# Optimization experiments

Measured on AMD Instinct MI355X. Metric: run time of the kernel, lower is better.

Reference implementation:

```python
import math
import jax, jax.numpy as jnp
import numpy as np

D = 256       # d_model
R = 64        # low-rank bottleneck
E = 3         # num experts
KS = (1, 3, 5)
EPS = 0.1     # sinkhorn epsilon
ITERS = 10    # sinkhorn iterations


def _ln(x, g, b):
    m = jnp.mean(x, -1, keepdims=True)
    v = jnp.mean((x - m) ** 2, -1, keepdims=True)
    return (x - m) * jax.lax.rsqrt(v + 1e-5) * g + b


def _gelu(x):
    return jax.nn.gelu(x, approximate=False)  # torch nn.GELU default (erf)


def setup_inputs() -> dict:
    key = jax.random.key(0)
    ks = jax.random.split(key, 12)
    s = 0.02
    B, Lt, La = 16, 1024, 2048
    return {
        "text_feat": jax.random.normal(ks[0], (B, Lt, D), jnp.float32),
        "audio_feat": jax.random.normal(ks[1], (B, La, D), jnp.float32),
        # shared OT projection (LayerNorm + Linear, shared across modalities)
        "ln_g": jnp.ones((D,), jnp.float32),
        "ln_b": jnp.zeros((D,), jnp.float32),
        "W_sh": jax.random.normal(ks[2], (D, D), jnp.float32) * s,
        "b_sh": jnp.zeros((D,), jnp.float32),
        # contradiction router: Linear(d+1->d) GELU Linear(d->E)
        "Wr1": jax.random.normal(ks[3], (D, D + 1), jnp.float32) * s,
        "br1": jnp.zeros((D,), jnp.float32),
        "Wr2": jax.random.normal(ks[4], (E, D), jnp.float32) * s,
        "br2": jnp.zeros((E,), jnp.float32),
        # 3 low-rank conv experts (stacked where shapes match)
        "down_W": jax.random.normal(ks[5], (E, R, D), jnp.float32) * s,
        "down_b": jnp.zeros((E, R), jnp.float32),
        "conv_w1": jax.random.normal(ks[6], (R, R, 1), jnp.float32) * s,
        "conv_w3": jax.random.normal(ks[7], (R, R, 3), jnp.float32) * s,
        "conv_w5": jax.random.normal(ks[8], (R, R, 5), jnp.float32) * s,
        "conv_b": jnp.zeros((E, R), jnp.float32),
        "up_W": jax.random.normal(ks[9], (E, D, R), jnp.float32) * s,
        "up_b": jnp.zeros((E, D), jnp.float32),
        "en_g": jnp.ones((E, D), jnp.float32),
        "en_b": jnp.zeros((E, D), jnp.float32),
    }


def reference(text_feat, audio_feat, ln_g, ln_b, W_sh, b_sh, Wr1, br1, Wr2, br2,
              down_W, down_b, conv_w1, conv_w3, conv_w5, conv_b, up_W, up_b, en_g, en_b):
    B, Lt, _ = text_feat.shape
    La = audio_feat.shape[1]

    # ---- shared projection (dropout = identity at eval) ----
    Tp = _ln(text_feat, ln_g, ln_b) @ W_sh.T + b_sh      # [B,Lt,D]
    Ap = _ln(audio_feat, ln_g, ln_b) @ W_sh.T + b_sh     # [B,La,D]

    # ---- cosine cost ----
    Tn = Tp / jnp.maximum(jnp.linalg.norm(Tp, axis=-1, keepdims=True), 1e-12)
    An = Ap / jnp.maximum(jnp.linalg.norm(Ap, axis=-1, keepdims=True), 1e-12)
    cost = 1.0 - jnp.einsum('bmd,bnd->bmn', Tn, An)      # [B,Lt,La]

    # ---- log-domain Sinkhorn (uniform marginals, no masks) ----
    log_K = -cost / (EPS + 1e-8)
    log_mu = jnp.full((B, Lt), -math.log(Lt), jnp.float32)
    log_nu = jnp.full((B, La), -math.log(La), jnp.float32)
    lu = jnp.zeros((B, Lt), jnp.float32)
    lv = jnp.zeros((B, La), jnp.float32)
    for _ in range(ITERS):
        lu = log_mu - jax.scipy.special.logsumexp(log_K + lv[:, None, :], axis=-1)
        lu = jnp.nan_to_num(jnp.clip(lu, -1e9, 1e9), nan=0.0, posinf=1e9, neginf=-1e9)
        lv = log_nu - jax.scipy.special.logsumexp(log_K + lu[:, :, None], axis=1)
        lv = jnp.nan_to_num(jnp.clip(lv, -1e9, 1e9), nan=0.0, posinf=1e9, neginf=-1e9)
    pi = jnp.exp(lu[:, :, None] + log_K + lv[:, None, :])
    pi = jnp.nan_to_num(pi, nan=0.0, posinf=1.0, neginf=0.0)  # [B,Lt,La]

    A_al = jnp.einsum('bmn,bnd->bmd', pi, Ap)            # [B,Lt,D]
    S = jnp.sum(Tp * A_al, -1)                           # [B,Lt]
    resid = jnp.abs(Tp - A_al)                           # [B,Lt,D]

    # ---- contradiction router ----
    rin = jnp.concatenate([S[..., None], resid], -1)     # [B,Lt,D+1]
    G = jax.nn.softmax(_gelu(rin @ Wr1.T + br1) @ Wr2.T + br2, axis=-1)  # [B,Lt,E]

    # ---- multi-scale low-rank conv MoE over contradiction residual ----
    convs = (conv_w1, conv_w3, conv_w5)
    x = resid
    out = jnp.zeros_like(Tp)
    for e in range(E):
        h = _gelu(x @ down_W[e].T + down_b[e])           # [B,Lt,R]
        k = convs[e].shape[-1]
        pad = (k - 1) // 2
        hc = jax.lax.conv_general_dilated(
            h.transpose(0, 2, 1), convs[e], (1,), [(pad, pad)],
            dimension_numbers=('NCH', 'OIH', 'NCH')) + conv_b[e][None, :, None]
        h = _gelu(hc).transpose(0, 2, 1)                 # [B,Lt,R]
        h = h @ up_W[e].T + up_b[e]                      # [B,Lt,D]
        eo = _ln(h + x, en_g[e], en_b[e])
        out = out + G[..., e:e + 1] * eo
    return out
```

## Files before the change

kernel.cpp:

```cpp
#include <hip/hip_runtime.h>
#include <cstdio>

#define D_ 256
#define LT 1024
#define LA 2048
#define NB 16
#define RR_ 64
#define NRT (NB*LT)
#define NRA (NB*LA)

#define DECQ  (-0.080645161f)
#define DECQ2 (-0.11634637f)

typedef short bf16x8 __attribute__((ext_vector_type(8)));
typedef float f32x4 __attribute__((ext_vector_type(4)));

__device__ __forceinline__ float gelu_f(float x) {
    return 0.5f * x * (1.0f + erff(x * 0.70710678118654752f));
}
__device__ __forceinline__ unsigned short f2bf(float f) {
    union { float f; unsigned int i; } c; c.f = f;
    unsigned int x = c.i;
    return (unsigned short)((x + 0x7fffu + ((x >> 16) & 1u)) >> 16);
}

__global__ __launch_bounds__(256) void k_prep_all(
    const float* __restrict__ W_sh, const float* __restrict__ down_W,
    const float* __restrict__ up_W, const float* __restrict__ Wr1,
    unsigned short* __restrict__ Wb, unsigned short* __restrict__ dWb,
    unsigned short* __restrict__ uWb, unsigned short* __restrict__ Wr1b)
{
    int i = blockIdx.x * 256 + threadIdx.x;
    if (i < 65536) Wb[i] = f2bf(W_sh[i]);
    else if (i < 114688) { int j = i - 65536; dWb[j] = f2bf(down_W[j]); }
    else if (i < 163840) { int j = i - 114688; uWb[j] = f2bf(up_W[j]); }
    else { int j = i - 163840; int n = j >> 8, k = j & 255; Wr1b[j] = f2bf(Wr1[(long)n * 257 + 1 + k]); }
}

__global__ __launch_bounds__(256) void k_lnproj_mfma(
    const float* __restrict__ X, const float* __restrict__ g, const float* __restrict__ bln,
    const unsigned short* __restrict__ Wb, const float* __restrict__ bsh,
    float* __restrict__ Pf, unsigned short* __restrict__ Nb)
{
    __shared__ short xb[64][264];
    __shared__ short Bs[256][40];
    int tid = threadIdx.x;
    long row0 = (long)blockIdx.x * 64;
    {
        int lane = tid & 31, rg = tid >> 5;
        float4 ga = *(const float4*)(g + lane * 8);
        float4 gb2 = *(const float4*)(g + lane * 8 + 4);
        float4 ba = *(const float4*)(bln + lane * 8);
        float4 bb2 = *(const float4*)(bln + lane * 8 + 4);
        for (int it = 0; it < 8; it++) {
            int r = it * 8 + rg;
            const float4* xp4 = (const float4*)(X + (row0 + r) * D_);
            float4 a = xp4[lane * 2], b = xp4[lane * 2 + 1];
            float s = a.x + a.y + a.z + a.w + b.x + b.y + b.z + b.w;
#pragma unroll
            for (int off = 16; off >= 1; off >>= 1) s += __shfl_xor(s, off);
            float mean = s * (1.0f / 256.0f);
            float q = (a.x - mean) * (a.x - mean) + (a.y - mean) * (a.y - mean)
                    + (a.z - mean) * (a.z - mean) + (a.w - mean) * (a.w - mean)
                    + (b.x - mean) * (b.x - mean) + (b.y - mean) * (b.y - mean)
                    + (b.z - mean) * (b.z - mean) + (b.w - mean) * (b.w - mean);
#pragma unroll
            for (int off = 16; off >= 1; off >>= 1) q += __shfl_xor(q, off);
            float ivar = rsqrtf(q * (1.0f / 256.0f) + 1e-5f);
            unsigned int u0 = f2bf((a.x - mean) * ivar * ga.x + ba.x);
            unsigned int u1 = f2bf((a.y - mean) * ivar * ga.y + ba.y);
            unsigned int u2 = f2bf((a.z - mean) * ivar * ga.z + ba.z);
            unsigned int u3 = f2bf((a.w - mean) * ivar * ga.w + ba.w);
            unsigned int u4 = f2bf((b.x - mean) * ivar * gb2.x + bb2.x);
            unsigned int u5 = f2bf((b.y - mean) * ivar * gb2.y + bb2.y);
            unsigned int u6 = f2bf((b.z - mean) * ivar * gb2.z + bb2.z);
            unsigned int u7 = f2bf((b.w - mean) * ivar * gb2.w + bb2.w);
            int4 pv;
            pv.x = (int)(u0 | (u1 << 16)); pv.y = (int)(u2 | (u3 << 16));
            pv.z = (int)(u4 | (u5 << 16)); pv.w = (int)(u6 | (u7 << 16));
            *(int4*)&xb[r][lane * 8] = pv;
        }
    }
    __syncthreads();
    int wid = tid >> 6, lane = tid & 63;
    int l15 = lane & 15, kq = lane >> 4;
    int m_local = wid * 16;
    f32x4 acc[16];
#pragma unroll
    for (int j = 0; j < 16; j++) acc[j] = (f32x4){0.f, 0.f, 0.f, 0.f};
    for (int kt = 0; kt < 8; kt++) {
        int k0 = kt * 32;
#pragma unroll
        for (int h = 0; h < 4; h++) {
            int idx = tid + 256 * h;
            int n = idx >> 2, qc = idx & 3;
            *(int4*)&Bs[n][qc * 8] = *(const int4*)(Wb + (long)n * D_ + k0 + qc * 8);
        }
        __syncthreads();
        bf16x8 af = *(const bf16x8*)&xb[m_local + l15][k0 + kq * 8];
#pragma unroll
        for (int j = 0; j < 16; j++) {
            bf16x8 bf = *(const bf16x8*)&Bs[j * 16 + l15][kq * 8];
            acc[j] = __builtin_amdgcn_mfma_f32_16x16x32_bf16(af, bf, acc[j], 0, 0, 0);
        }
        __syncthreads();
    }
#pragma unroll
    for (int j = 0; j < 16; j++) {
        float bv = bsh[j * 16 + l15];
#pragma unroll
        for (int r = 0; r < 4; r++) acc[j][r] += bv;
    }
    float sq[4] = {0.f, 0.f, 0.f, 0.f};
#pragma unroll
    for (int j = 0; j < 16; j++)
#pragma unroll
        for (int r = 0; r < 4; r++) sq[r] += acc[j][r] * acc[j][r];
#pragma unroll
    for (int off = 8; off >= 1; off >>= 1) {
#pragma unroll
        for (int r = 0; r < 4; r++) sq[r] += __shfl_xor(sq[r], off);
    }
    float rinv[4];
#pragma unroll
    for (int r = 0; r < 4; r++) rinv[r] = 1.0f / fmaxf(sqrtf(sq[r]), 1e-12f);
#pragma unroll
    for (int j = 0; j < 16; j++) {
        int col = j * 16 + l15;
#pragma unroll
        for (int r = 0; r < 4; r++) {
            long m = row0 + m_local + kq * 4 + r;
            if (Pf) Pf[m * D_ + col] = acc[j][r];
            Nb[m * D_ + col] = f2bf(acc[j][r] * rinv[r]);
        }
    }
}

__global__ __launch_bounds__(256) void k_transpose_bf(
    const unsigned short* __restrict__ Anb, unsigned short* __restrict__ ApbT)
{
    __shared__ short t[64][68];
    int b = blockIdx.x;
    int n0 = blockIdx.y * 64;
    int d0 = blockIdx.z * 64;
    int tid = threadIdx.x;
#pragma unroll
    for (int h = 0; h < 2; h++) {
        int c = tid + 256 * h;
        int nr = c >> 3, ch = c & 7;
        *(int4*)&t[nr][ch * 8] = *(const int4*)(Anb + ((long)b * LA + n0 + nr) * D_ + d0 + ch * 8);
    }
    __syncthreads();
#pragma unroll
    for (int h = 0; h < 2; h++) {
        int c = tid + 256 * h;
        int d = c >> 3, nch = c & 7;
        unsigned short v[8];
#pragma unroll
        for (int k = 0; k < 8; k++) v[k] = (unsigned short)t[nch * 8 + k][d];
        int4 ov;
        ov.x = (int)((unsigned int)v[0] | ((unsigned int)v[1] << 16));
        ov.y = (int)((unsigned int)v[2] | ((unsigned int)v[3] << 16));
        ov.z = (int)((unsigned int)v[4] | ((unsigned int)v[5] << 16));
        ov.w = (int)((unsigned int)v[6] | ((unsigned int)v[7] << 16));
        *(int4*)(ApbT + ((long)b * D_ + d0 + d) * LA + n0 + nch * 8) = ov;
    }
}

__global__ __launch_bounds__(256) void k_cost_mfma(
    const unsigned short* __restrict__ Tnb, const unsigned short* __restrict__ Anb,
    unsigned char* __restrict__ logK8, unsigned char* __restrict__ logK8T)
{
    __shared__ short sm[2][128][48];
    short (*As)[48] = sm[0];
    short (*Bs)[48] = sm[1];
    unsigned char* tile = (unsigned char*)sm;
    int b = blockIdx.x;
    int m_blk = blockIdx.y * 128, n_blk = blockIdx.z * 128;
    int tid = threadIdx.x;
    int wid = tid >> 6, lane = tid & 63;
    int l15 = lane & 15, kq = lane >> 4;
    int wm0 = (wid >> 1) * 64, wn0 = (wid & 1) * 64;
    const unsigned short* Ab = Tnb + ((long)b * LT + m_blk) * D_;
    const unsigned short* Bb = Anb + ((long)b * LA + n_blk) * D_;
    f32x4 acc[4][4];
#pragma unroll
    for (int i = 0; i < 4; i++)
#pragma unroll
        for (int j = 0; j < 4; j++) acc[i][j] = (f32x4){0.f, 0.f, 0.f, 0.f};
    for (int kt = 0; kt < 8; kt++) {
        int k0 = kt * 32;
#pragma unroll
        for (int h = 0; h < 2; h++) {
            int idx = tid + 256 * h;
            int row = idx >> 2, ch = idx & 3;
            *(int4*)&As[row][ch * 8] = *(const int4*)(Ab + (long)row * D_ + k0 + ch * 8);
            *(int4*)&Bs[row][ch * 8] = *(const int4*)(Bb + (long)row * D_ + k0 + ch * 8);
        }
        __syncthreads();
        bf16x8 af[4], bfv[4];
#pragma unroll
        for (int i = 0; i < 4; i++) af[i] = *(const bf16x8*)&As[wm0 + i * 16 + l15][kq * 8];
#pragma unroll
        for (int j = 0; j < 4; j++) bfv[j] = *(const bf16x8*)&Bs[wn0 + j * 16 + l15][kq * 8];
#pragma unroll
        for (int i = 0; i < 4; i++)
#pragma unroll
            for (int j = 0; j < 4; j++)
                acc[i][j] = __builtin_amdgcn_mfma_f32_16x16x32_bf16(af[i], bfv[j], acc[i][j], 0, 0, 0);
        __syncthreads();
    }
#pragma unroll
    for (int i = 0; i < 4; i++) {
#pragma unroll
        for (int j = 0; j < 4; j++) {
            int n = wn0 + j * 16 + l15;
            long base = ((long)b * LT + m_blk + wm0 + i * 16 + kq * 4) * (long)LA + n_blk + n;
            unsigned int pk = 0;
#pragma unroll
            for (int r = 0; r < 4; r++) {
                float q = rintf((1.0f - acc[i][j][r]) * 124.0f);
                q = fminf(fmaxf(q, 0.0f), 255.0f);
                unsigned int qb = (unsigned int)q;
                pk |= qb << (8 * r);
                logK8[base + (long)r * LA] = (unsigned char)qb;
            }
            *(unsigned int*)&tile[n * 144 + wm0 + i * 16 + kq * 4] = pk;
        }
    }
    __syncthreads();
#pragma unroll
    for (int h = 0; h < 4; h++) {
        int idx = tid + 256 * h;
        int row = idx >> 3, ch = idx & 7;
        int4 v = *(const int4*)&tile[row * 144 + ch * 16];
        *(int4*)(logK8T + ((long)b * LA + n_blk + row) * (long)LT + m_blk + ch * 16) = v;
    }
}

__global__ __launch_bounds__(256) void k_rowlse2(
    const unsigned char* __restrict__ logK8, const float* __restrict__ lv2,
    float* __restrict__ lu2, int first)
{
    __shared__ float red[8][4];
    int b = blockIdx.x & 15;
    int mseg = blockIdx.x >> 4;
    int tid = threadIdx.x;
    int wid = tid >> 6, lane = tid & 63;
    float lvv[8] = {0.f, 0.f, 0.f, 0.f, 0.f, 0.f, 0.f, 0.f};
    if (!first) {
        const float* lvp = lv2 + (long)b * LA + tid * 8;
        float4 l0 = *(const float4*)lvp, l1 = *(const float4*)(lvp + 4);
        lvv[0] = l0.x; lvv[1] = l0.y; lvv[2] = l0.z; lvv[3] = l0.w;
        lvv[4] = l1.x; lvv[5] = l1.y; lvv[6] = l1.z; lvv[7] = l1.w;
    }
    const unsigned char* p = logK8 + ((long)b * LT + mseg * 8) * (long)LA + tid * 8;
#pragma unroll
    for (int r = 0; r < 8; r++) {
        uint2 w = *(const uint2*)(p + (long)r * LA);
        unsigned int w0 = w.x, w1 = w.y;
        float s = 0.f;
        s += exp2f(fmaf((float)(w0 & 0xffu),         DECQ2, lvv[0]));
        s += exp2f(fmaf((float)((w0 >> 8) & 0xffu),  DECQ2, lvv[1]));
        s += exp2f(fmaf((float)((w0 >> 16) & 0xffu), DECQ2, lvv[2]));
        s += exp2f(fmaf((float)(w0 >> 24),           DECQ2, lvv[3]));
        s += exp2f(fmaf((float)(w1 & 0xffu),         DECQ2, lvv[4]));
        s += exp2f(fmaf((float)((w1 >> 8) & 0xffu),  DECQ2, lvv[5]));
        s += exp2f(fmaf((float)((w1 >> 16) & 0xffu), DECQ2, lvv[6]));
        s += exp2f(fmaf((float)(w1 >> 24),           DECQ2, lvv[7]));
#pragma unroll
        for (int off = 32; off >= 1; off >>= 1) s += __shfl_xor(s, off);
        if (lane == 0) red[r][wid] = s;
    }
    __syncthreads();
    if (tid < 8) {
        float s = red[tid][0] + red[tid][1] + red[tid][2] + red[tid][3];
        lu2[(long)b * LT + mseg * 8 + tid] = -10.0f - __log2f(s);
    }
}

__global__ __launch_bounds__(256) void k_collse2(
    const unsigned char* __restrict__ logK8T, const float* __restrict__ lu2,
    float* __restrict__ lv2, int final_)
{
    __shared__ float red[16][2];
    int b = blockIdx.x & 15;
    int nseg = blockIdx.x >> 4;
    int tid = threadIdx.x;
    int t7 = tid & 127;
    int g = tid >> 7;
    int wid = tid >> 6, lane = tid & 63;
    const float* lup = lu2 + (long)b * LT + t7 * 8;
    float4 l0 = *(const float4*)lup, l1 = *(const float4*)(lup + 4);
    float lus[8] = {l0.x, l0.y, l0.z, l0.w, l1.x, l1.y, l1.z, l1.w};
    const unsigned char* base = logK8T + ((long)b * LA + nseg * 16) * (long)LT + t7 * 8;
#pragma unroll
    for (int it = 0; it < 8; it++) {
        int c = it * 2 + g;
        uint2 w = *(const uint2*)(base + (long)c * LT);
        unsigned int w0 = w.x, w1 = w.y;
        float s = 0.f;
        s += exp2f(fmaf((float)(w0 & 0xffu),         DECQ2, lus[0]));
        s += exp2f(fmaf((float)((w0 >> 8) & 0xffu),  DECQ2, lus[1]));
        s += exp2f(fmaf((float)((w0 >> 16) & 0xffu), DECQ2, lus[2]));
        s += exp2f(fmaf((float)(w0 >> 24),           DECQ2, lus[3]));
        s += exp2f(fmaf((float)(w1 & 0xffu),         DECQ2, lus[4]));
        s += exp2f(fmaf((float)((w1 >> 8) & 0xffu),  DECQ2, lus[5]));
        s += exp2f(fmaf((float)((w1 >> 16) & 0xffu), DECQ2, lus[6]));
        s += exp2f(fmaf((float)(w1 >> 24),           DECQ2, lus[7]));
#pragma unroll
        for (int off = 32; off >= 1; off >>= 1) s += __shfl_xor(s, off);
        if (lane == 0) red[c][wid & 1] = s;
    }
    __syncthreads();
    if (tid < 16) {
        float s = red[tid][0] + red[tid][1];
        lv2[(long)b * LA + nseg * 16 + tid] = final_ ? (0.00048828125f / s)
                                                     : (-11.0f - __log2f(s));
    }
}

__global__ __launch_bounds__(256) void k_scale_ev(
    unsigned short* __restrict__ ApbT, const float* __restrict__ ev)
{
    int b = blockIdx.x;
    int d = blockIdx.y;
    int tid = threadIdx.x;
    long off = ((long)b * D_ + d) * (long)LA + tid * 8;
    int4 v = *(const int4*)(ApbT + off);
    const float* ep = ev + (long)b * LA + tid * 8;
    float4 e0 = *(const float4*)ep, e1 = *(const float4*)(ep + 4);
    unsigned int u[4] = {(unsigned int)v.x, (unsigned int)v.y, (unsigned int)v.z, (unsigned int)v.w};
    float ee[8] = {e0.x, e0.y, e0.z, e0.w, e1.x, e1.y, e1.z, e1.w};
    unsigned int o[4];
#pragma unroll
    for (int k = 0; k < 4; k++) {
        float lo = __uint_as_float(u[k] << 16) * ee[2 * k];
        float hi = __uint_as_float(u[k] & 0xffff0000u) * ee[2 * k + 1];
        o[k] = (unsigned int)f2bf(lo) | ((unsigned int)f2bf(hi) << 16);
    }
    int4 ov; ov.x = (int)o[0]; ov.y = (int)o[1]; ov.z = (int)o[2]; ov.w = (int)o[3];
    *(int4*)(ApbT + off) = ov;
}

__global__ __launch_bounds__(256) void k_pi2(
    const unsigned char* __restrict__ logK8, const unsigned short* __restrict__ Av,
    const float* __restrict__ lu2, float* __restrict__ Apart)
{
    __shared__ short As[64][48];
    __shared__ short Bs[256][48];
    __shared__ float eus[64];
    int b = blockIdx.x;
    int kh = blockIdx.y;
    int m_blk = blockIdx.z * 64;
    int nbase = kh * 1024;
    int tid = threadIdx.x;
    if (tid < 64) eus[tid] = exp2f(lu2[(long)b * LT + m_blk + tid]);
    int wid = tid >> 6, lane = tid & 63;
    int l15 = lane & 15, kq = lane >> 4;
    int wm0 = (wid & 1) * 32, wd0 = (wid >> 1) * 128;
    f32x4 acc[2][8];
#pragma unroll
    for (int i = 0; i < 2; i++)
#pragma unroll
        for (int j = 0; j < 8; j++) acc[i][j] = (f32x4){0.f, 0.f, 0.f, 0.f};
    const unsigned char* Kbase = logK8 + ((long)b * LT + m_blk) * (long)LA + nbase;
    const unsigned short* Bbase = Av + (long)b * D_ * (long)LA + nbase;
    int arow = tid >> 2, ac8 = (tid & 3) * 8;
    for (int kt = 0; kt < 32; kt++) {
        int n0 = kt * 32;
        {
            uint2 raw = *(const uint2*)(Kbase + (long)arow * LA + n0 + ac8);
            unsigned int w0 = raw.x, w1 = raw.y;
            unsigned int o0 = f2bf(exp2f((float)(w0 & 0xffu) * DECQ2));
            unsigned int o1 = f2bf(exp2f((float)((w0 >> 8) & 0xffu) * DECQ2));
            unsigned int o2 = f2bf(exp2f((float)((w0 >> 16) & 0xffu) * DECQ2));
            unsigned int o3 = f2bf(exp2f((float)(w0 >> 24) * DECQ2));
            unsigned int o4 = f2bf(exp2f((float)(w1 & 0xffu) * DECQ2));
            unsigned int o5 = f2bf(exp2f((float)((w1 >> 8) & 0xffu) * DECQ2));
            unsigned int o6 = f2bf(exp2f((float)((w1 >> 16) & 0xffu) * DECQ2));
            unsigned int o7 = f2bf(exp2f((float)(w1 >> 24) * DECQ2));
            int4 ov;
            ov.x = (int)(o0 | (o1 << 16)); ov.y = (int)(o2 | (o3 << 16));
            ov.z = (int)(o4 | (o5 << 16)); ov.w = (int)(o6 | (o7 << 16));
            *(int4*)&As[arow][ac8] = ov;
        }
#pragma unroll
        for (int h = 0; h < 4; h++) {
            int idx = tid + 256 * h;
            int row = idx >> 2, ch = idx & 3;
            *(int4*)&Bs[row][ch * 8] = *(const int4*)(Bbase + (long)row * LA + n0 + ch * 8);
        }
        __syncthreads();
        bf16x8 af[2], bfv[8];
        af[0] = *(const bf16x8*)&As[wm0 + l15][kq * 8];
        af[1] = *(const bf16x8*)&As[wm0 + 16 + l15][kq * 8];
#pragma unroll
        for (int j = 0; j < 8; j++) bfv[j] = *(const bf16x8*)&Bs[wd0 + j * 16 + l15][kq * 8];
#pragma unroll
        for (int i = 0; i < 2; i++)
#pragma unroll
            for (int j = 0; j < 8; j++)
                acc[i][j] = __builtin_amdgcn_mfma_f32_16x16x32_bf16(af[i], bfv[j], acc[i][j], 0, 0, 0);
        __syncthreads();
    }
    float* dst = Apart + (long)kh * (NB * (long)LT * D_);
#pragma unroll
    for (int i = 0; i < 2; i++) {
#pragma unroll
        for (int r = 0; r < 4; r++) {
            int rloc = wm0 + i * 16 + kq * 4 + r;
            float eu = eus[rloc];
            int m = m_blk + rloc;
            long obase = ((long)b * LT + m) * D_;
#pragma unroll
            for (int j = 0; j < 8; j++)
                dst[obase + wd0 + j * 16 + l15] = acc[i][j][r] * eu;
        }
    }
}

__global__ __launch_bounds__(256) void k_sresid(
    const float* __restrict__ Tp, const float* __restrict__ Apart,
    float* __restrict__ resid, unsigned short* __restrict__ residb, float* __restrict__ S)
{
    __shared__ float red[4];
    int b = blockIdx.x & 15;
    int m = blockIdx.x >> 4;
    long row = (long)b * LT + m;
    int tid = threadIdx.x;
    long idx = row * D_ + tid;
    float t = Tp[idx];
    float a = Apart[idx] + Apart[idx + (long)NB * LT * D_];
    float rr = fabsf(t - a);
    resid[idx] = rr;
    residb[idx] = f2bf(rr);
    float p = t * a;
#pragma unroll
    for (int off = 32; off >= 1; off >>= 1) p += __shfl_xor(p, off);
    if ((tid & 63) == 0) red[tid >> 6] = p;
    __syncthreads();
    if (tid == 0) S[row] = red[0] + red[1] + red[2] + red[3];
}

__global__ __launch_bounds__(256) void k_router_fused(
    const unsigned short* __restrict__ residb, const unsigned short* __restrict__ Wr1b,
    const float* __restrict__ Wr1, const float* __restrict__ br1,
    const float* __restrict__ S, const float* __restrict__ Wr2,
    const float* __restrict__ br2, float* __restrict__ G)
{
    __shared__ short xb[16][264];
    __shared__ short Bs[256][40];
    __shared__ float red[4][3][16];
    int tid = threadIdx.x;
    long row0 = (long)blockIdx.x * 16;
#pragma unroll
    for (int h = 0; h < 2; h++) {
        int idx = tid + 256 * h;
        int row = idx >> 5, ch = idx & 31;
        *(int4*)&xb[row][ch * 8] = *(const int4*)(residb + (row0 + row) * D_ + ch * 8);
    }
    __syncthreads();
    int wid = tid >> 6, lane = tid & 63;
    int l15 = lane & 15, kq = lane >> 4;
    f32x4 acc[4];
#pragma unroll
    for (int j = 0; j < 4; j++) acc[j] = (f32x4){0.f, 0.f, 0.f, 0.f};
    for (int kt = 0; kt < 8; kt++) {
        int k0 = kt * 32;
#pragma unroll
        for (int h = 0; h < 4; h++) {
            int idx = tid + 256 * h;
            int n = idx >> 2, qc = idx & 3;
            *(int4*)&Bs[n][qc * 8] = *(const int4*)(Wr1b + (long)n * D_ + k0 + qc * 8);
        }
        __syncthreads();
        bf16x8 af = *(const bf16x8*)&xb[l15][k0 + kq * 8];
#pragma unroll
        for (int j = 0; j < 4; j++) {
            bf16x8 bf = *(const bf16x8*)&Bs[wid * 64 + j * 16 + l15][kq * 8];
            acc[j] = __builtin_amdgcn_mfma_f32_16x16x32_bf16(af, bf, acc[j], 0, 0, 0);
        }
        __syncthreads();
    }
    float sv[4];
#pragma unroll
    for (int r = 0; r < 4; r++) sv[r] = S[row0 + kq * 4 + r];
    float le[3][4] = {};
#pragma unroll
    for (int j = 0; j < 4; j++) {
        int col = wid * 64 + j * 16 + l15;
        float w0 = Wr1[(long)col * 257];
        float bv = br1[col];
        float w2a = Wr2[col], w2b = Wr2[256 + col], w2c = Wr2[512 + col];
#pragma unroll
        for (int r = 0; r < 4; r++) {
            float hv = gelu_f(acc[j][r] + sv[r] * w0 + bv);
            le[0][r] += hv * w2a;
            le[1][r] += hv * w2b;
            le[2][r] += hv * w2c;
        }
    }
#pragma unroll
    for (int off = 8; off >= 1; off >>= 1)
#pragma unroll
        for (int e = 0; e < 3; e++)
#pragma unroll
            for (int r = 0; r < 4; r++) le[e][r] += __shfl_xor(le[e][r], off);
    if (l15 == 0) {
#pragma unroll
        for (int e = 0; e < 3; e++)
#pragma unroll
            for (int r = 0; r < 4; r++) red[wid][e][kq * 4 + r] = le[e][r];
    }
    __syncthreads();
    if (tid < 16) {
        float L0 = red[0][0][tid] + red[1][0][tid] + red[2][0][tid] + red[3][0][tid] + br2[0];
        float L1 = red[0][1][tid] + red[1][1][tid] + red[2][1][tid] + red[3][1][tid] + br2[1];
        float L2 = red[0][2][tid] + red[1][2][tid] + red[2][2][tid] + red[3][2][tid] + br2[2];
        float mx = fmaxf(L0, fmaxf(L1, L2));
        float e0 = __expf(L0 - mx), e1 = __expf(L1 - mx), e2 = __expf(L2 - mx);
        float inv = 1.0f / (e0 + e1 + e2);
        long m = row0 + tid;
        G[m] = e0 * inv; G[NRT + m] = e1 * inv; G[2 * NRT + m] = e2 * inv;
    }
}

__global__ __launch_bounds__(256) void k_down_mfma(
    const unsigned short* __restrict__ residb, const unsigned short* __restrict__ dWb,
    const float* __restrict__ db, float* __restrict__ hall)
{
    __shared__ short xb[64][264];
    __shared__ short Bs[64][40];
    int tid = threadIdx.x;
    int e = blockIdx.y;
    int b = blockIdx.x & 15;
    int mseg = blockIdx.x >> 4;
    long row0 = (long)b * LT + mseg * 64;
    const unsigned short* dWe = dWb + (long)e * RR_ * D_;
    float* h = hall + (long)e * NRT * RR_;
#pragma unroll
    for (int hh = 0; hh < 8; hh++) {
        int idx = tid + 256 * hh;
        int row = idx >> 5, ch = idx & 31;
        *(int4*)&xb[row][ch * 8] = *(const int4*)(residb + (row0 + row) * D_ + ch * 8);
    }
    __syncthreads();
    int wid = tid >> 6, lane = tid & 63;
    int l15 = lane & 15, kq = lane >> 4;
    int m_local = wid * 16;
    f32x4 acc[4];
#pragma unroll
    for (int j = 0; j < 4; j++) acc[j] = (f32x4){0.f, 0.f, 0.f, 0.f};
    for (int kt = 0; kt < 8; kt++) {
        int k0 = kt * 32;
        {
            int n = tid >> 2, qc = tid & 3;
            *(int4*)&Bs[n][qc * 8] = *(const int4*)(dWe + (long)n * D_ + k0 + qc * 8);
        }
        __syncthreads();
        bf16x8 af = *(const bf16x8*)&xb[m_local + l15][k0 + kq * 8];
#pragma unroll
        for (int j = 0; j < 4; j++) {
            bf16x8 bf = *(const bf16x8*)&Bs[j * 16 + l15][kq * 8];
            acc[j] = __builtin_amdgcn_mfma_f32_16x16x32_bf16(af, bf, acc[j], 0, 0, 0);
        }
        __syncthreads();
    }
#pragma unroll
    for (int j = 0; j < 4; j++) {
        int col = j * 16 + l15;
        float bv = db[e * RR_ + col];
#pragma unroll
        for (int r = 0; r < 4; r++) {
            long m = row0 + m_local + kq * 4 + r;
            h[m * RR_ + col] = gelu_f(acc[j][r] + bv);
        }
    }
}

__global__ __launch_bounds__(256) void k_conv_all(
    const float* __restrict__ hall, const float* __restrict__ cw1,
    const float* __restrict__ cw3, const float* __restrict__ cw5,
    const float* __restrict__ conv_b, unsigned short* __restrict__ hcbb)
{
    __shared__ float hs[68][68];
    __shared__ float wt[64][64];
    int e = blockIdx.y;
    const float* w = (e == 0) ? cw1 : ((e == 1) ? cw3 : cw5);
    int ksz = (e == 0) ? 1 : ((e == 1) ? 3 : 5);
    const float* h = hall + (long)e * NRT * RR_;
    unsigned short* hcb = hcbb + (long)e * NRT * RR_;
    const float* cb = conv_b + e * 64;
    int b = blockIdx.x & 15;
    int m0 = (blockIdx.x >> 4) * 64;
    int tid = threadIdx.x;
    int pad = (ksz - 1) >> 1;
    for (int idx = tid; idx < 68 * 16; idx += 256) {
        int mr = idx >> 4, i4 = idx & 15;
        int mm = m0 - 2 + mr;
        float4 vv = { 0.f, 0.f, 0.f, 0.f };
        if (mm >= 0 && mm < LT) vv = *(const float4*)(h + ((long)b * LT + mm) * RR_ + i4 * 4);
        *(float4*)&hs[mr][i4 * 4] = vv;
    }
    int tx = tid & 15, ty = tid >> 4;
    float acc[4][4] = {};
    for (int t = 0; t < ksz; t++) {
        __syncthreads();
        for (int idx = tid; idx < 4096; idx += 256) {
            int i = idx & 63, j = idx >> 6;
            wt[i][j] = w[(long)j * RR_ * ksz + i * ksz + t];
        }
        __syncthreads();
        int roff = ty * 4 + 2 + t - pad;
        for (int i4 = 0; i4 < 16; i4++) {
            float4 h0 = *(const float4*)&hs[roff + 0][i4 * 4];
            float4 h1 = *(const float4*)&hs[roff + 1][i4 * 4];
            float4 h2 = *(const float4*)&hs[roff + 2][i4 * 4];
            float4 h3 = *(const float4*)&hs[roff + 3][i4 * 4];
            float hh[4][4] = { { h0.x, h0.y, h0.z, h0.w }, { h1.x, h1.y, h1.z, h1.w },
                               { h2.x, h2.y, h2.z, h2.w }, { h3.x, h3.y, h3.z, h3.w } };
#pragma unroll
            for (int s = 0; s < 4; s++) {
                float4 wv = *(const float4*)&wt[i4 * 4 + s][tx * 4];
#pragma unroll
                for (int r = 0; r < 4; r++) {
                    acc[r][0] += hh[r][s] * wv.x;
                    acc[r][1] += hh[r][s] * wv.y;
                    acc[r][2] += hh[r][s] * wv.z;
                    acc[r][3] += hh[r][s] * wv.w;
                }
            }
        }
    }
    float4 bb = *(const float4*)(cb + tx * 4);
#pragma unroll
    for (int r = 0; r < 4; r++) {
        long m = (long)b * LT + m0 + ty * 4 + r;
        unsigned long long pv =
              (unsigned long long)f2bf(gelu_f(acc[r][0] + bb.x))
            | ((unsigned long long)f2bf(gelu_f(acc[r][1] + bb.y)) << 16)
            | ((unsigned long long)f2bf(gelu_f(acc[r][2] + bb.z)) << 32)
            | ((unsigned long long)f2bf(gelu_f(acc[r][3] + bb.w)) << 48);
        *(unsigned long long*)(hcb + m * RR_ + tx * 4) = pv;
    }
}

__global__ __launch_bounds__(256) void k_up3(
    const unsigned short* __restrict__ hcbb, const unsigned short* __restrict__ uWb,
    const float* __restrict__ up_b, const float* __restrict__ resid,
    const float* __restrict__ en_g, const float* __restrict__ en_b,
    const float* __restrict__ G, float* __restrict__ out)
{
    __shared__ short hs[64][88];
    __shared__ short Bs[256][40];
    int tid = threadIdx.x;
    int b = blockIdx.x & 15;
    int mseg = blockIdx.x >> 4;
    long row0 = (long)b * LT + mseg * 64;
    int wid = tid >> 6, lane = tid & 63;
    int l15 = lane & 15, kq = lane >> 4;
    int m_local = wid * 16;
    long mrow[4];
#pragma unroll
    for (int r = 0; r < 4; r++) mrow[r] = row0 + m_local + kq * 4 + r;
    f32x4 outacc[16];
#pragma unroll
    for (int j = 0; j < 16; j++) outacc[j] = (f32x4){0.f, 0.f, 0.f, 0.f};
    for (int e = 0; e < 3; e++) {
        __syncthreads();
        const unsigned short* hcb = hcbb + (long)e * NRT * RR_;
        const unsigned short* uWe = uWb + (long)e * 16384;
#pragma unroll
        for (int hh = 0; hh < 2; hh++) {
            int idx = tid + 256 * hh;
            int row = idx >> 3, ch = idx & 7;
            *(int4*)&hs[row][ch * 8] = *(const int4*)(hcb + (row0 + row) * RR_ + ch * 8);
        }
        f32x4 acc[16];
#pragma unroll
        for (int j = 0; j < 16; j++) acc[j] = (f32x4){0.f, 0.f, 0.f, 0.f};
        for (int kt = 0; kt < 2; kt++) {
            int k0 = kt * 32;
#pragma unroll
            for (int hh = 0; hh < 4; hh++) {
                int idx = tid + 256 * hh;
                int n = idx >> 2, qc = idx & 3;
                *(int4*)&Bs[n][qc * 8] = *(const int4*)(uWe + (long)n * RR_ + k0 + qc * 8);
            }
            __syncthreads();
            bf16x8 af = *(const bf16x8*)&hs[m_local + l15][k0 + kq * 8];
#pragma unroll
            for (int j = 0; j < 16; j++) {
                bf16x8 bf = *(const bf16x8*)&Bs[j * 16 + l15][kq * 8];
                acc[j] = __builtin_amdgcn_mfma_f32_16x16x32_bf16(af, bf, acc[j], 0, 0, 0);
            }
            __syncthreads();
        }
        const float* ub = up_b + e * 256;
#pragma unroll
        for (int j = 0; j < 16; j++) {
            int col = j * 16 + l15;
            float bv = ub[col];
#pragma unroll
            for (int r = 0; r < 4; r++)
                acc[j][r] += bv + resid[mrow[r] * D_ + col];
        }
        float s[4] = {0.f, 0.f, 0.f, 0.f};
#pragma unroll
        for (int j = 0; j < 16; j++)
#pragma unroll
            for (int r = 0; r < 4; r++) s[r] += acc[j][r];
#pragma unroll
        for (int off = 8; off >= 1; off >>= 1)
#pragma unroll
            for (int r = 0; r < 4; r++) s[r] += __shfl_xor(s[r], off);
        float mn[4];
#pragma unroll
        for (int r = 0; r < 4; r++) mn[r] = s[r] * (1.0f / 256.0f);
        float q[4] = {0.f, 0.f, 0.f, 0.f};
#pragma unroll
        for (int j = 0; j < 16; j++)
#pragma unroll
            for (int r = 0; r < 4; r++) { float d = acc[j][r] - mn[r]; q[r] += d * d; }
#pragma unroll
        for (int off = 8; off >= 1; off >>= 1)
#pragma unroll
            for (int r = 0; r < 4; r++) q[r] += __shfl_xor(q[r], off);
        float iv[4], gv[4];
#pragma unroll
        for (int r = 0; r < 4; r++) {
            iv[r] = rsqrtf(q[r] * (1.0f / 256.0f) + 1e-5f);
            gv[r] = G[(long)e * NRT + mrow[r]];
        }
        const float* eg = en_g + e * 256;
        const float* eb = en_b + e * 256;
#pragma unroll
        for (int j = 0; j < 16; j++) {
            int col = j * 16 + l15;
            float egc = eg[col], ebc = eb[col];
#pragma unroll
            for (int r = 0; r < 4; r++)
                outacc[j][r] += gv[r] * ((acc[j][r] - mn[r]) * iv[r] * egc + ebc);
        }
    }
#pragma unroll
    for (int j = 0; j < 16; j++) {
        int col = j * 16 + l15;
#pragma unroll
        for (int r = 0; r < 4; r++)
            out[mrow[r] * D_ + col] = outacc[j][r];
    }
}

extern "C" void kernel_launch(void* const* d_in, const int* in_sizes, int n_in,
                              void* d_out, int out_size, void* d_ws, size_t ws_size,
                              hipStream_t stream)
{
    const float* text   = (const float*)d_in[0];
    const float* audio  = (const float*)d_in[1];
    const float* ln_g   = (const float*)d_in[2];
    const float* ln_b   = (const float*)d_in[3];
    const float* W_sh   = (const float*)d_in[4];
    const float* b_sh   = (const float*)d_in[5];
    const float* Wr1    = (const float*)d_in[6];
    const float* br1    = (const float*)d_in[7];
    const float* Wr2    = (const float*)d_in[8];
    const float* br2    = (const float*)d_in[9];
    const float* down_W = (const float*)d_in[10];
    const float* down_b = (const float*)d_in[11];
    const float* cw1    = (const float*)d_in[12];
    const float* cw3    = (const float*)d_in[13];
    const float* cw5    = (const float*)d_in[14];
    const float* conv_b = (const float*)d_in[15];
    const float* up_W   = (const float*)d_in[16];
    const float* up_b   = (const float*)d_in[17];
    const float* en_g   = (const float*)d_in[18];
    const float* en_b   = (const float*)d_in[19];

    float* ws = (float*)d_ws;
    float*          Tp    = ws;
    unsigned short* Tnb   = (unsigned short*)(ws + 4194304);
    unsigned short* Anb   = (unsigned short*)(ws + 6291456);
    unsigned short* ApbT  = (unsigned short*)(ws + 10485760);
    unsigned char*  logK8 = (unsigned char*)(ws + 14680064);
    float*          Apart = ws + 23068672;
    float*          resid = ws + 31457280;
    unsigned short* residb= (unsigned short*)(ws + 35651584);
    float*          lu2   = ws + 37748736;
    float*          lv2   = ws + 37765120;
    float*          Sb    = ws + 37797888;
    float*          Gb    = ws + 37814272;
    unsigned short* Wb    = (unsigned short*)(ws + 37863424);
    unsigned short* dWb   = (unsigned short*)(ws + 37896192);
    unsigned short* uWb   = (unsigned short*)(ws + 37920768);
    unsigned short* Wr1b  = (unsigned short*)(ws + 37945344);
    size_t need_bytes = (size_t)37978112 * 4;
    if (ws_size < need_bytes) {
        fprintf(stderr, "kernel_launch: ws_size %zu < needed %zu\n", ws_size, need_bytes);
        return;
    }
    float*          hall = ws + 14680064;
    unsigned short* hcbb = (unsigned short*)(ws + 17825792);
    unsigned char*  logK8T = (unsigned char*)(ws + 23068672);

    k_prep_all<<<896, 256, 0, stream>>>(W_sh, down_W, up_W, Wr1, Wb, dWb, uWb, Wr1b);
    k_lnproj_mfma<<<NRT / 64, 256, 0, stream>>>(text, ln_g, ln_b, Wb, b_sh, Tp, Tnb);
    k_lnproj_mfma<<<NRA / 64, 256, 0, stream>>>(audio, ln_g, ln_b, Wb, b_sh, nullptr, Anb);
    k_transpose_bf<<<dim3(NB, LA / 64, D_ / 64), 256, 0, stream>>>(Anb, ApbT);
    k_cost_mfma<<<dim3(NB, LT / 128, LA / 128), 256, 0, stream>>>(Tnb, Anb, logK8, logK8T);
    for (int it = 0; it < 10; it++) {
        k_rowlse2<<<NRT / 8, 256, 0, stream>>>(logK8, lv2, lu2, it == 0 ? 1 : 0);
        k_collse2<<<NB * (LA / 16), 256, 0, stream>>>(logK8T, lu2, lv2, it == 9 ? 1 : 0);
    }
    k_scale_ev<<<dim3(NB, D_), 256, 0, stream>>>(ApbT, lv2);
    k_pi2<<<dim3(NB, 2, LT / 64), 256, 0, stream>>>(logK8, ApbT, lu2, Apart);
    k_sresid<<<NRT, 256, 0, stream>>>(Tp, Apart, resid, residb, Sb);
    k_router_fused<<<NRT / 16, 256, 0, stream>>>(residb, Wr1b, Wr1, br1, Sb, Wr2, br2, Gb);
    k_down_mfma<<<dim3(NRT / 64, 3), 256, 0, stream>>>(residb, dWb, down_b, hall);
    k_conv_all<<<dim3(NRT / 64, 3), 256, 0, stream>>>(hall, cw1, cw3, cw5, conv_b, hcbb);
    k_up3<<<NRT / 64, 256, 0, stream>>>(hcbb, uWb, up_b, resid, en_g, en_b, Gb, (float*)d_out);
}
```

Before: 581.6 us.

## Restructure Sinkhorn LSE kernels for more parallelism and use hardware exp2/bf16 pack

The row and column log-sum-exp kernels now give each block fewer rows or columns, 2 rows and 4 columns instead of 8 and 16. Each thread loads 16 bytes with a single vector load, so the grid has more blocks and more loads are in flight. exp2f is replaced with the raw v_exp_f32 builtin and the software bf16 rounding with v_cvt_pk_bf16_f32 in the scale and pi kernels. The LDS row stride in k_pi2 is padded from 48 to 56 to change the bank-conflict pattern. The fast exp skips denormal handling, and the extra blocks mean lv2/lu2 vectors are re-read more times.

```diff
diff --git a/kernel.cpp b/kernel.cpp
--- a/kernel.cpp
+++ b/kernel.cpp
@@ -22,6 +22,18 @@
     union { float f; unsigned int i; } c; c.f = f;
     unsigned int x = c.i;
     return (unsigned short)((x + 0x7fffu + ((x >> 16) & 1u)) >> 16);
+}
+__device__ __forceinline__ float exp2_fast(float x) {
+#if __has_builtin(__builtin_amdgcn_exp2f)
+    return __builtin_amdgcn_exp2f(x);
+#else
+    float r; asm("v_exp_f32 %0, %1" : "=v"(r) : "v"(x)); return r;
+#endif
+}
+__device__ __forceinline__ unsigned int cvt_pk_bf16(float lo, float hi) {
+    unsigned int r;
+    asm("v_cvt_pk_bf16_f32 %0, %1, %2" : "=v"(r) : "v"(lo), "v"(hi));
+    return r;
 }
 
 __global__ __launch_bounds__(256) void k_prep_all(
@@ -238,85 +250,85 @@
     }
 }
 
-__global__ __launch_bounds__(256) void k_rowlse2(
+__global__ __launch_bounds__(256) void k_rowlse3(
     const unsigned char* __restrict__ logK8, const float* __restrict__ lv2,
     float* __restrict__ lu2, int first)
 {
-    __shared__ float red[8][4];
+    __shared__ float red[2][2];
     int b = blockIdx.x & 15;
     int mseg = blockIdx.x >> 4;
     int tid = threadIdx.x;
-    int wid = tid >> 6, lane = tid & 63;
-    float lvv[8] = {0.f, 0.f, 0.f, 0.f, 0.f, 0.f, 0.f, 0.f};
+    int row = tid >> 7;
+    int ln = tid & 127;
+    float lvv[16];
     if (!first) {
-        const float* lvp = lv2 + (long)b * LA + tid * 8;
-        float4 l0 = *(const float4*)lvp, l1 = *(const float4*)(lvp + 4);
-        lvv[0] = l0.x; lvv[1] = l0.y; lvv[2] = l0.z; lvv[3] = l0.w;
-        lvv[4] = l1.x; lvv[5] = l1.y; lvv[6] = l1.z; lvv[7] = l1.w;
-    }
-    const unsigned char* p = logK8 + ((long)b * LT + mseg * 8) * (long)LA + tid * 8;
-#pragma unroll
-    for (int r = 0; r < 8; r++) {
-        uint2 w = *(const uint2*)(p + (long)r * LA);
-        unsigned int w0 = w.x, w1 = w.y;
-        float s = 0.f;
-        s += exp2f(fmaf((float)(w0 & 0xffu),         DECQ2, lvv[0]));
-        s += exp2f(fmaf((float)((w0 >> 8) & 0xffu),  DECQ2, lvv[1]));
-        s += exp2f(fmaf((float)((w0 >> 16) & 0xffu), DECQ2, lvv[2]));
-        s += exp2f(fmaf((float)(w0 >> 24),           DECQ2, lvv[3]));
-        s += exp2f(fmaf((float)(w1 & 0xffu),         DECQ2, lvv[4]));
-        s += exp2f(fmaf((float)((w1 >> 8) & 0xffu),  DECQ2, lvv[5]));
-        s += exp2f(fmaf((float)((w1 >> 16) & 0xffu), DECQ2, lvv[6]));
-        s += exp2f(fmaf((float)(w1 >> 24),           DECQ2, lvv[7]));
-#pragma unroll
-        for (int off = 32; off >= 1; off >>= 1) s += __shfl_xor(s, off);
-        if (lane == 0) red[r][wid] = s;
-    }
+        const float* lvp = lv2 + (long)b * LA + ln * 16;
+#pragma unroll
+        for (int k = 0; k < 4; k++) {
+            float4 l = *(const float4*)(lvp + k * 4);
+            lvv[k * 4 + 0] = l.x; lvv[k * 4 + 1] = l.y;
+            lvv[k * 4 + 2] = l.z; lvv[k * 4 + 3] = l.w;
+        }
+    } else {
+#pragma unroll
+        for (int k = 0; k < 16; k++) lvv[k] = 0.f;
+    }
+    const unsigned char* p = logK8 + ((long)b * LT + mseg * 2 + row) * (long)LA + ln * 16;
+    uint4 w = *(const uint4*)p;
+    unsigned int ws4[4] = {w.x, w.y, w.z, w.w};
+    float s = 0.f;
+#pragma unroll
+    for (int k = 0; k < 4; k++) {
+        unsigned int u = ws4[k];
+        s += exp2_fast(fmaf((float)(u & 0xffu),         DECQ2, lvv[k * 4 + 0]));
+        s += exp2_fast(fmaf((float)((u >> 8) & 0xffu),  DECQ2, lvv[k * 4 + 1]));
+        s += exp2_fast(fmaf((float)((u >> 16) & 0xffu), DECQ2, lvv[k * 4 + 2]));
+        s += exp2_fast(fmaf((float)(u >> 24),           DECQ2, lvv[k * 4 + 3]));
+    }
+#pragma unroll
+    for (int off = 32; off >= 1; off >>= 1) s += __shfl_xor(s, off);
+    if ((tid & 63) == 0) red[row][(tid >> 6) & 1] = s;
     __syncthreads();
-    if (tid < 8) {
-        float s = red[tid][0] + red[tid][1] + red[tid][2] + red[tid][3];
-        lu2[(long)b * LT + mseg * 8 + tid] = -10.0f - __log2f(s);
-    }
-}
-
-__global__ __launch_bounds__(256) void k_collse2(
+    if (tid < 2) {
+        float sr = red[tid][0] + red[tid][1];
+        lu2[(long)b * LT + mseg * 2 + tid] = -10.0f - __log2f(sr);
+    }
+}
+
+__global__ __launch_bounds__(256) void k_collse3(
     const unsigned char* __restrict__ logK8T, const float* __restrict__ lu2,
     float* __restrict__ lv2, int final_)
 {
-    __shared__ float red[16][2];
     int b = blockIdx.x & 15;
     int nseg = blockIdx.x >> 4;
     int tid = threadIdx.x;
-    int t7 = tid & 127;
-    int g = tid >> 7;
-    int wid = tid >> 6, lane = tid & 63;
-    const float* lup = lu2 + (long)b * LT + t7 * 8;
-    float4 l0 = *(const float4*)lup, l1 = *(const float4*)(lup + 4);
-    float lus[8] = {l0.x, l0.y, l0.z, l0.w, l1.x, l1.y, l1.z, l1.w};
-    const unsigned char* base = logK8T + ((long)b * LA + nseg * 16) * (long)LT + t7 * 8;
-#pragma unroll
-    for (int it = 0; it < 8; it++) {
-        int c = it * 2 + g;
-        uint2 w = *(const uint2*)(base + (long)c * LT);
-        unsigned int w0 = w.x, w1 = w.y;
-        float s = 0.f;
-        s += exp2f(fmaf((float)(w0 & 0xffu),         DECQ2, lus[0]));
-        s += exp2f(fmaf((float)((w0 >> 8) & 0xffu),  DECQ2, lus[1]));
-        s += exp2f(fmaf((float)((w0 >> 16) & 0xffu), DECQ2, lus[2]));
-        s += exp2f(fmaf((float)(w0 >> 24),           DECQ2, lus[3]));
-        s += exp2f(fmaf((float)(w1 & 0xffu),         DECQ2, lus[4]));
-        s += exp2f(fmaf((float)((w1 >> 8) & 0xffu),  DECQ2, lus[5]));
-        s += exp2f(fmaf((float)((w1 >> 16) & 0xffu), DECQ2, lus[6]));
-        s += exp2f(fmaf((float)(w1 >> 24),           DECQ2, lus[7]));
-#pragma unroll
-        for (int off = 32; off >= 1; off >>= 1) s += __shfl_xor(s, off);
-        if (lane == 0) red[c][wid & 1] = s;
-    }
-    __syncthreads();
-    if (tid < 16) {
-        float s = red[tid][0] + red[tid][1];
-        lv2[(long)b * LA + nseg * 16 + tid] = final_ ? (0.00048828125f / s)
-                                                     : (-11.0f - __log2f(s));
+    int wv = tid >> 6, lane = tid & 63;
+    int c = nseg * 4 + wv;
+    float lus[16];
+    const float* lup = lu2 + (long)b * LT + lane * 16;
+#pragma unroll
+    for (int k = 0; k < 4; k++) {
+        float4 l = *(const float4*)(lup + k * 4);
+        lus[k * 4 + 0] = l.x; lus[k * 4 + 1] = l.y;
+        lus[k * 4 + 2] = l.z; lus[k * 4 + 3] = l.w;
+    }
+    const unsigned char* p = logK8T + ((long)b * LA + c) * (long)LT + lane * 16;
+    uint4 w = *(const uint4*)p;
+    unsigned int ws4[4] = {w.x, w.y, w.z, w.w};
+    float s = 0.f;
+#pragma unroll
+    for (int k = 0; k < 4; k++) {
+        unsigned int u = ws4[k];
+        s += exp2_fast(fmaf((float)(u & 0xffu),         DECQ2, lus[k * 4 + 0]));
+        s += exp2_fast(fmaf((float)((u >> 8) & 0xffu),  DECQ2, lus[k * 4 + 1]));
+        s += exp2_fast(fmaf((float)((u >> 16) & 0xffu), DECQ2, lus[k * 4 + 2]));
+        s += exp2_fast(fmaf((float)(u >> 24),           DECQ2, lus[k * 4 + 3]));
+    }
+#pragma unroll
+    for (int off = 32; off >= 1; off >>= 1) s += __shfl_xor(s, off);
+    if (lane == 0) {
+        lv2[(long)b * LA + c] = final_ ? (0.00048828125f / s)
+                                       : (-11.0f - __log2f(s));
     }
 }
 
@@ -337,7 +349,7 @@
     for (int k = 0; k < 4; k++) {
         float lo = __uint_as_float(u[k] << 16) * ee[2 * k];
         float hi = __uint_as_float(u[k] & 0xffff0000u) * ee[2 * k + 1];
-        o[k] = (unsigned int)f2bf(lo) | ((unsigned int)f2bf(hi) << 16);
+        o[k] = cvt_pk_bf16(lo, hi);
     }
     int4 ov; ov.x = (int)o[0]; ov.y = (int)o[1]; ov.z = (int)o[2]; ov.w = (int)o[3];
     *(int4*)(ApbT + off) = ov;
@@ -347,15 +359,15 @@
     const unsigned char* __restrict__ logK8, const unsigned short* __restrict__ Av,
     const float* __restrict__ lu2, float* __restrict__ Apart)
 {
-    __shared__ short As[64][48];
-    __shared__ short Bs[256][48];
+    __shared__ short As[64][56];
+    __shared__ short Bs[256][56];
     __shared__ float eus[64];
     int b = blockIdx.x;
     int kh = blockIdx.y;
     int m_blk = blockIdx.z * 64;
     int nbase = kh * 1024;
     int tid = threadIdx.x;
-    if (tid < 64) eus[tid] = exp2f(lu2[(long)b * LT + m_blk + tid]);
+    if (tid < 64) eus[tid] = exp2_fast(lu2[(long)b * LT + m_blk + tid]);
     int wid = tid >> 6, lane = tid & 63;
     int l15 = lane & 15, kq = lane >> 4;
     int wm0 = (wid & 1) * 32, wd0 = (wid >> 1) * 128;
@@ -372,17 +384,17 @@
         {
             uint2 raw = *(const uint2*)(Kbase + (long)arow * LA + n0 + ac8);
             unsigned int w0 = raw.x, w1 = raw.y;
-            unsigned int o0 = f2bf(exp2f((float)(w0 & 0xffu) * DECQ2));
-            unsigned int o1 = f2bf(exp2f((float)((w0 >> 8) & 0xffu) * DECQ2));
-            unsigned int o2 = f2bf(exp2f((float)((w0 >> 16) & 0xffu) * DECQ2));
-            unsigned int o3 = f2bf(exp2f((float)(w0 >> 24) * DECQ2));
-            unsigned int o4 = f2bf(exp2f((float)(w1 & 0xffu) * DECQ2));
-            unsigned int o5 = f2bf(exp2f((float)((w1 >> 8) & 0xffu) * DECQ2));
-            unsigned int o6 = f2bf(exp2f((float)((w1 >> 16) & 0xffu) * DECQ2));
-            unsigned int o7 = f2bf(exp2f((float)(w1 >> 24) * DECQ2));
+            float e0 = exp2_fast((float)(w0 & 0xffu) * DECQ2);
+            float e1 = exp2_fast((float)((w0 >> 8) & 0xffu) * DECQ2);
+            float e2 = exp2_fast((float)((w0 >> 16) & 0xffu) * DECQ2);
+            float e3 = exp2_fast((float)(w0 >> 24) * DECQ2);
+            float e4 = exp2_fast((float)(w1 & 0xffu) * DECQ2);
+            float e5 = exp2_fast((float)((w1 >> 8) & 0xffu) * DECQ2);
+            float e6 = exp2_fast((float)((w1 >> 16) & 0xffu) * DECQ2);
+            float e7 = exp2_fast((float)(w1 >> 24) * DECQ2);
             int4 ov;
-            ov.x = (int)(o0 | (o1 << 16)); ov.y = (int)(o2 | (o3 << 16));
-            ov.z = (int)(o4 | (o5 << 16)); ov.w = (int)(o6 | (o7 << 16));
+            ov.x = (int)cvt_pk_bf16(e0, e1); ov.y = (int)cvt_pk_bf16(e2, e3);
+            ov.z = (int)cvt_pk_bf16(e4, e5); ov.w = (int)cvt_pk_bf16(e6, e7);
             *(int4*)&As[arow][ac8] = ov;
         }
 #pragma unroll
@@ -810,8 +822,8 @@
     k_transpose_bf<<<dim3(NB, LA / 64, D_ / 64), 256, 0, stream>>>(Anb, ApbT);
     k_cost_mfma<<<dim3(NB, LT / 128, LA / 128), 256, 0, stream>>>(Tnb, Anb, logK8, logK8T);
     for (int it = 0; it < 10; it++) {
-        k_rowlse2<<<NRT / 8, 256, 0, stream>>>(logK8, lv2, lu2, it == 0 ? 1 : 0);
-        k_collse2<<<NB * (LA / 16), 256, 0, stream>>>(logK8T, lu2, lv2, it == 9 ? 1 : 0);
+        k_rowlse3<<<NRT / 2, 256, 0, stream>>>(logK8, lv2, lu2, it == 0 ? 1 : 0);
+        k_collse3<<<NB * (LA / 4), 256, 0, stream>>>(logK8T, lu2, lv2, it == 9 ? 1 : 0);
     }
     k_scale_ev<<<dim3(NB, D_), 256, 0, stream>>>(ApbT, lv2);
     k_pi2<<<dim3(NB, 2, LT / 64), 256, 0, stream>>>(logK8, ApbT, lu2, Apart);
```

Measured after the change: 534.2 us. 1.09x faster.
